# Performance work log

Measured on AMD Instinct MI355X. Metric: run time of the kernel, lower is better.

Reference implementation:

```python
import jax, jax.numpy as jnp
import numpy as np

# Neighbor offsets (dy, dx) for kernels j=0..7. Each torch conv with a
# [-1 at neighbor, +1 at center] 3x3 kernel and padding=1 equals
# x - shift(x, offset) with zero-padded borders.
_OFFSETS = [(0, -1), (1, -1), (1, 0), (1, 1), (0, 1), (-1, 1), (-1, 0), (-1, -1)]
_EPS = 1e-5


def setup_inputs() -> dict:
    key = jax.random.key(0)
    x = jax.random.normal(key, (32, 1, 1024, 1024), dtype=jnp.float32)
    return {"x": x}


def _ltpe_forward(x):
    B, C, H, W = x.shape
    xp = jnp.pad(x, ((0, 0), (0, 0), (1, 1), (1, 1)))  # zero border, matches conv padding=1
    out = jnp.zeros_like(x)
    for j, (dy, dx) in enumerate(_OFFSETS):
        nb = jax.lax.dynamic_slice(xp, (0, 0, 1 + dy, 1 + dx), (B, C, H, W))
        diff = x - nb                      # conv output for kernel j
        out = out + ((diff + 1.0) * 0.5) * (float(2 ** j) / 255.0)
    # InstanceNorm2d(1): normalize over (H, W) per sample/channel, no affine,
    # biased variance, eps=1e-5.
    mean = jnp.mean(out, axis=(2, 3), keepdims=True)
    var = jnp.var(out, axis=(2, 3), keepdims=True)
    return (out - mean) * jax.lax.rsqrt(var + _EPS)


def reference(x):
    return _ltpe_forward(x)
```

## Files before the change

### kernel.cpp

```cpp
#include <hip/hip_runtime.h>


#define HH 1024
#define WW 1024
#define HW (HH * WW)
#define NIMG 32
#define NBLK1 64
#define RPB1 (HH / NBLK1)
#define NBLK2 32
#define RPB2 (HH / NBLK2)
#define TPB 256

typedef float vfloat4 __attribute__((ext_vector_type(4)));
typedef float vfloat4u __attribute__((ext_vector_type(4), aligned(4)));
typedef float vfloat2u __attribute__((ext_vector_type(2), aligned(4)));

__device__ __forceinline__ void compute_y(const float* up, const float* mid,
                                          const float* dn, float* y) {
    const float w0 = 1.f / 255.f,  w1 = 2.f / 255.f,  w2 = 4.f / 255.f,
                w3 = 8.f / 255.f,  w4 = 16.f / 255.f, w5 = 32.f / 255.f,
                w6 = 64.f / 255.f, w7 = 128.f / 255.f;
#pragma unroll
    for (int k = 0; k < 4; ++k) {
        float s = w0 * mid[k] + w4 * mid[k + 2]
                + w1 * dn[k]  + w2 * dn[k + 1] + w3 * dn[k + 2]
                + w7 * up[k]  + w6 * up[k + 1] + w5 * up[k + 2];
        y[k] = mid[k + 1] - s;
    }
}

__device__ __forceinline__ void load_row_g(const float* __restrict__ base,
                                           int r, int c, float* buf) {
    if (r < 0 || r >= HH) {
#pragma unroll
        for (int k = 0; k < 6; ++k) buf[k] = 0.f;
        return;
    }
    const float* p = base + (size_t)r * WW + 4 * c;
    const bool notfirst = (c > 0);
    const bool notlast = (c < TPB - 1);
    const vfloat4u a = *reinterpret_cast<const vfloat4u*>(p - (notfirst ? 1 : 0));
    const vfloat2u b = *reinterpret_cast<const vfloat2u*>(p + (notlast ? 3 : 2));
    buf[0] = notfirst ? a.x : 0.f;
    buf[1] = notfirst ? a.y : a.x;
    buf[2] = notfirst ? a.z : a.y;
    buf[3] = notfirst ? a.w : a.z;
    buf[4] = notlast ? b.x : b.y;
    buf[5] = notlast ? b.y : 0.f;
}

__global__ __launch_bounds__(TPB) void ltpe_stats(const float* __restrict__ x,
                                                  float* __restrict__ partials) {
    const int img = blockIdx.x / NBLK1;
    const int blk = blockIdx.x % NBLK1;
    const int c = threadIdx.x;
    const float* base = x + (size_t)img * HW;
    const int r0 = blk * RPB1;

    float buf[4][6];
    load_row_g(base, r0 - 1, c, buf[0]);
    load_row_g(base, r0,     c, buf[1]);
    load_row_g(base, r0 + 1, c, buf[2]);
    load_row_g(base, r0 + 2, c, buf[3]);

    float s = 0.f, ss = 0.f;
#pragma unroll
    for (int i = 0; i < RPB1; ++i) {
        const int r = r0 + i;
        float y[4];
        compute_y(buf[i & 3], buf[(i + 1) & 3], buf[(i + 2) & 3], y);
#pragma unroll
        for (int k = 0; k < 4; ++k) { s += y[k]; ss = fmaf(y[k], y[k], ss); }
        if (i + 2 < RPB1)
            load_row_g(base, r + 3, c, buf[i & 3]);
    }

#pragma unroll
    for (int off = 32; off > 0; off >>= 1) {
        s += __shfl_down(s, off);
        ss += __shfl_down(ss, off);
    }
    __shared__ float sh[8];
    const int wave = threadIdx.x >> 6;
    const int lane = threadIdx.x & 63;
    if (lane == 0) { sh[wave] = s; sh[4 + wave] = ss; }
    __syncthreads();
    if (threadIdx.x == 0) {
        partials[img * NBLK1 + blk] = sh[0] + sh[1] + sh[2] + sh[3];
        partials[NIMG * NBLK1 + img * NBLK1 + blk] = sh[4] + sh[5] + sh[6] + sh[7];
    }
}

__global__ __launch_bounds__(TPB) void ltpe_norm(const float* __restrict__ x,
                                                 const float* __restrict__ partials,
                                                 float* __restrict__ out) {
    const int img = blockIdx.x / NBLK2;
    const int blk = blockIdx.x % NBLK2;
    const int c = threadIdx.x;
    const float* base = x + (size_t)img * HW;
    const int r0 = blk * RPB2;

    float buf[4][6];
    load_row_g(base, r0 - 1, c, buf[0]);
    load_row_g(base, r0,     c, buf[1]);
    load_row_g(base, r0 + 1, c, buf[2]);
    load_row_g(base, r0 + 2, c, buf[3]);

    __shared__ float sh_stats[2];
    if (threadIdx.x < 64) {
        const int lane = threadIdx.x;
        double S = (double)partials[img * NBLK1 + lane];
        double SS = (double)partials[NIMG * NBLK1 + img * NBLK1 + lane];
#pragma unroll
        for (int off = 32; off > 0; off >>= 1) {
            S += __shfl_down(S, off);
            SS += __shfl_down(SS, off);
        }
        if (lane == 0) {
            const double N = (double)HW;
            const double m = S / N;
            const double var = SS / N - m * m;
            sh_stats[0] = (float)m;
            sh_stats[1] = (float)(1.0 / sqrt(var + 4e-5));
        }
    }
    __syncthreads();
    const float mean = sh_stats[0];
    const float scale = sh_stats[1];

    float* obase = out + (size_t)img * HW;

#pragma unroll
    for (int i = 0; i < RPB2; ++i) {
        const int r = r0 + i;
        float y[4];
        compute_y(buf[i & 3], buf[(i + 1) & 3], buf[(i + 2) & 3], y);
        vfloat4 o;
        o.x = (y[0] - mean) * scale;
        o.y = (y[1] - mean) * scale;
        o.z = (y[2] - mean) * scale;
        o.w = (y[3] - mean) * scale;
        __builtin_nontemporal_store(
            o, reinterpret_cast<vfloat4*>(obase + (size_t)r * WW) + c);
        if (i + 2 < RPB2)
            load_row_g(base, r + 3, c, buf[i & 3]);
    }
}

extern "C" void kernel_launch(void* const* d_in, const int* in_sizes, int n_in,
                              void* d_out, int out_size, void* d_ws, size_t ws_size,
                              hipStream_t stream) {
    const float* x = (const float*)d_in[0];
    float* out = (float*)d_out;
    float* partials = (float*)d_ws;

    ltpe_stats<<<NIMG * NBLK1, TPB, 0, stream>>>(x, partials);
    ltpe_norm<<<NIMG * NBLK2, TPB, 0, stream>>>(x, partials, out);
}
```

Before: 69.79 us.

## Write unnormalized stencil in stats pass, then normalize output in place

The first pass now stores the stencil result to the output buffer while accumulating statistics. The second pass reads that buffer back and applies a scale-and-bias in place instead of rereading the input and recomputing the stencil. This removes stencil recomputation and halo loads but adds an extra full-size write plus a read-modify-write of the output, raising total memory traffic.

```diff
diff --git a/kernel.cpp b/kernel.cpp
--- a/kernel.cpp
+++ b/kernel.cpp
@@ -7,8 +7,8 @@
 #define NIMG 32
 #define NBLK1 64
 #define RPB1 (HH / NBLK1)
-#define NBLK2 32
-#define RPB2 (HH / NBLK2)
+#define NBLK2 64
+#define EPB2 (HW / NBLK2)
 #define TPB 256
 
 typedef float vfloat4 __attribute__((ext_vector_type(4)));
@@ -49,12 +49,14 @@
     buf[5] = notlast ? b.y : 0.f;
 }
 
-__global__ __launch_bounds__(TPB) void ltpe_stats(const float* __restrict__ x,
-                                                  float* __restrict__ partials) {
+__global__ __launch_bounds__(TPB) void ltpe_stencil(const float* __restrict__ x,
+                                                    float* __restrict__ partials,
+                                                    float* __restrict__ out) {
     const int img = blockIdx.x / NBLK1;
     const int blk = blockIdx.x % NBLK1;
     const int c = threadIdx.x;
     const float* base = x + (size_t)img * HW;
+    float* obase = out + (size_t)img * HW;
     const int r0 = blk * RPB1;
 
     float buf[4][6];
@@ -71,6 +73,9 @@
         compute_y(buf[i & 3], buf[(i + 1) & 3], buf[(i + 2) & 3], y);
 #pragma unroll
         for (int k = 0; k < 4; ++k) { s += y[k]; ss = fmaf(y[k], y[k], ss); }
+        vfloat4 o;
+        o.x = y[0]; o.y = y[1]; o.z = y[2]; o.w = y[3];
+        reinterpret_cast<vfloat4*>(obase + (size_t)r * WW)[c] = o;
         if (i + 2 < RPB1)
             load_row_g(base, r + 3, c, buf[i & 3]);
     }
@@ -91,20 +96,10 @@
     }
 }
 
-__global__ __launch_bounds__(TPB) void ltpe_norm(const float* __restrict__ x,
-                                                 const float* __restrict__ partials,
-                                                 float* __restrict__ out) {
+__global__ __launch_bounds__(TPB) void ltpe_norm_ip(float* __restrict__ out,
+                                                    const float* __restrict__ partials) {
     const int img = blockIdx.x / NBLK2;
     const int blk = blockIdx.x % NBLK2;
-    const int c = threadIdx.x;
-    const float* base = x + (size_t)img * HW;
-    const int r0 = blk * RPB2;
-
-    float buf[4][6];
-    load_row_g(base, r0 - 1, c, buf[0]);
-    load_row_g(base, r0,     c, buf[1]);
-    load_row_g(base, r0 + 1, c, buf[2]);
-    load_row_g(base, r0 + 2, c, buf[3]);
 
     __shared__ float sh_stats[2];
     if (threadIdx.x < 64) {
@@ -127,23 +122,25 @@
     __syncthreads();
     const float mean = sh_stats[0];
     const float scale = sh_stats[1];
+    const float bias = -mean * scale;
 
-    float* obase = out + (size_t)img * HW;
+    float* p = out + (size_t)img * HW + (size_t)blk * EPB2;
 
 #pragma unroll
-    for (int i = 0; i < RPB2; ++i) {
-        const int r = r0 + i;
-        float y[4];
-        compute_y(buf[i & 3], buf[(i + 1) & 3], buf[(i + 2) & 3], y);
-        vfloat4 o;
-        o.x = (y[0] - mean) * scale;
-        o.y = (y[1] - mean) * scale;
-        o.z = (y[2] - mean) * scale;
-        o.w = (y[3] - mean) * scale;
-        __builtin_nontemporal_store(
-            o, reinterpret_cast<vfloat4*>(obase + (size_t)r * WW) + c);
-        if (i + 2 < RPB2)
-            load_row_g(base, r + 3, c, buf[i & 3]);
+    for (int i = 0; i < EPB2 / (TPB * 8); ++i) {
+        const int idx = i * TPB * 8 + threadIdx.x * 8;
+        vfloat4 a = *reinterpret_cast<vfloat4*>(p + idx);
+        vfloat4 b = *reinterpret_cast<vfloat4*>(p + idx + 4);
+        a.x = fmaf(a.x, scale, bias);
+        a.y = fmaf(a.y, scale, bias);
+        a.z = fmaf(a.z, scale, bias);
+        a.w = fmaf(a.w, scale, bias);
+        b.x = fmaf(b.x, scale, bias);
+        b.y = fmaf(b.y, scale, bias);
+        b.z = fmaf(b.z, scale, bias);
+        b.w = fmaf(b.w, scale, bias);
+        *reinterpret_cast<vfloat4*>(p + idx) = a;
+        *reinterpret_cast<vfloat4*>(p + idx + 4) = b;
     }
 }
 
@@ -154,6 +151,6 @@
     float* out = (float*)d_out;
     float* partials = (float*)d_ws;
 
-    ltpe_stats<<<NIMG * NBLK1, TPB, 0, stream>>>(x, partials);
-    ltpe_norm<<<NIMG * NBLK2, TPB, 0, stream>>>(x, partials, out);
+    ltpe_stencil<<<NIMG * NBLK1, TPB, 0, stream>>>(x, partials, out);
+    ltpe_norm_ip<<<NIMG * NBLK2, TPB, 0, stream>>>(out, partials);
 }
```

Result: slower. 91.02 us (+30.4%).
